# Kernel tuning notes

Hardware: AMD Instinct MI355X
Metric: run time of the kernel (lower is better)

Reference implementation:

```python
import jax, jax.numpy as jnp
import numpy as np

D, H, DK, DF = 512, 8, 64, 2048  # dim, heads, head_dim, forward_dim
EPS = 1e-5


def _layernorm(x, g, b):
    mu = jnp.mean(x, axis=-1, keepdims=True)
    var = jnp.mean(jnp.square(x - mu), axis=-1, keepdims=True)
    return (x - mu) * jax.lax.rsqrt(var + EPS) * g + b


def setup_inputs() -> dict:
    key = jax.random.key(0)
    ks = jax.random.split(key, 16)
    B, S = 2, 2048
    s_in = 1.0 / np.sqrt(D)
    s_ff = 1.0 / np.sqrt(DF)
    s_cat = 1.0 / np.sqrt(H * DK)
    return {
        "x": jax.random.normal(ks[0], (B, S, D), jnp.float32),
        # per-head Q/K/V projections stacked over heads: [H, D, DK]
        "Wq": jax.random.uniform(ks[1], (H, D, DK), jnp.float32, -s_in, s_in),
        "bq": jax.random.uniform(ks[2], (H, DK), jnp.float32, -s_in, s_in),
        "Wk": jax.random.uniform(ks[3], (H, D, DK), jnp.float32, -s_in, s_in),
        "bk": jax.random.uniform(ks[4], (H, DK), jnp.float32, -s_in, s_in),
        "Wv": jax.random.uniform(ks[5], (H, D, DK), jnp.float32, -s_in, s_in),
        "bv": jax.random.uniform(ks[6], (H, DK), jnp.float32, -s_in, s_in),
        "Wo": jax.random.uniform(ks[7], (H * DK, D), jnp.float32, -s_cat, s_cat),
        "bo": jax.random.uniform(ks[8], (D,), jnp.float32, -s_cat, s_cat),
        "ln1_g": jnp.ones((D,), jnp.float32),
        "ln1_b": jnp.zeros((D,), jnp.float32),
        "W1": jax.random.uniform(ks[9], (D, DF), jnp.float32, -s_in, s_in),
        "b1": jax.random.uniform(ks[10], (DF,), jnp.float32, -s_in, s_in),
        "W2": jax.random.uniform(ks[11], (DF, D), jnp.float32, -s_ff, s_ff),
        "b2": jax.random.uniform(ks[12], (D,), jnp.float32, -s_ff, s_ff),
        "ln2_g": jnp.ones((D,), jnp.float32),
        "ln2_b": jnp.zeros((D,), jnp.float32),
    }


def reference(x, Wq, bq, Wk, bk, Wv, bv, Wo, bo, ln1_g, ln1_b, W1, b1, W2, b2, ln2_g, ln2_b):
    # Per-head projections, batched over heads: [B,H,S,DK]
    q = jnp.einsum('bsd,hdk->bhsk', x, Wq) + bq[None, :, None, :]
    k = jnp.einsum('bsd,hdk->bhsk', x, Wk) + bk[None, :, None, :]
    v = jnp.einsum('bsd,hdk->bhsk', x, Wv) + bv[None, :, None, :]
    scale = 1.0 / np.sqrt(DK)
    scores = jnp.einsum('bhsk,bhtk->bhst', q, k) * scale  # [B,H,S,S]
    attn = jax.nn.softmax(scores, axis=-1)
    o = jnp.einsum('bhst,bhtk->bhsk', attn, v)  # [B,H,S,DK]
    # concat heads (head order matches torch cat over ModuleList)
    B, _, S, _ = o.shape
    o = o.transpose(0, 2, 1, 3).reshape(B, S, H * DK)
    attn_out = o @ Wo + bo
    # Residual 1 (dropout = identity in eval): LN(x + sublayer(x))
    h = _layernorm(x + attn_out, ln1_g, ln1_b)
    # FeedForward + Residual 2
    ff = jax.nn.relu(h @ W1 + b1) @ W2 + b2
    return _layernorm(h + ff, ln2_g, ln2_b)
```

## Files before the change

kernel.cpp:

```cpp
#include <hip/hip_runtime.h>


#define Dm   512
#define Hh   8
#define DKk  64
#define DFf  2048
#define Bb   2
#define Ss   2048
#define Nn   4096

typedef __attribute__((ext_vector_type(8))) short short8;
typedef __attribute__((ext_vector_type(4))) float f32x4;
typedef __attribute__((ext_vector_type(4))) short short4v;

__device__ inline float bf2f(short s) {
    unsigned u = ((unsigned)(unsigned short)s) << 16;
    float f; __builtin_memcpy(&f, &u, 4); return f;
}
__device__ inline short f2bf(float f) {
    unsigned u; __builtin_memcpy(&u, &f, 4);
    u = (u + 0x7fff + ((u >> 16) & 1)) >> 16;
    return (short)u;
}
__device__ inline short cvt_elem(const void* p, long i, int f32flag) {
    if (f32flag) return f2bf(((const float*)p)[i]);
    return ((const short*)p)[i];
}
__device__ inline int detect_f32(const void* x) {
    const float* xf = (const float*)x;
    int ok = 0;
#pragma unroll
    for (int i = 0; i < 16; ++i) {
        float a = fabsf(xf[i]);
        ok += (a > 1e-8f && a < 1e4f) ? 1 : 0;
    }
    return ok >= 8;
}
__device__ inline void gload_lds16(const short* g, short* l) {
    __builtin_amdgcn_global_load_lds(
        (const __attribute__((address_space(1))) unsigned int*)g,
        (__attribute__((address_space(3))) unsigned int*)l, 16, 0, 0);
}

__global__ __launch_bounds__(256) void prep_kernel(
    const void* __restrict__ x, short* __restrict__ xb,
    const void* bq, const void* bk, const void* bv, const void* bo,
    const void* b1, const void* b2, const void* g1, const void* be1,
    const void* g2, const void* be2, short* __restrict__ smalls,
    const void* Wq, const void* Wk, const void* Wv,
    const void* Wo, const void* W1, const void* W2,
    short* __restrict__ WqkvT,
    short* __restrict__ WoT, short* __restrict__ W1T, short* __restrict__ W2T)
{
    const int f = detect_f32(x);
    int blk = blockIdx.x;
    if (blk < 512) {
        long base = (long)blk * 4096;
        for (int i = threadIdx.x; i < 4096; i += 256)
            xb[base + i] = cvt_elem(x, base + i, f);
        return;
    }
    if (blk == 512) {
        const void* srcs[10] = {bq, bk, bv, bo, b1, b2, g1, be1, g2, be2};
        const int   sz[10]   = {512, 512, 512, 512, 2048, 512, 512, 512, 512, 512};
        int off = 0;
        for (int j = 0; j < 10; ++j) {
            for (int i = threadIdx.x; i < sz[j]; i += 256)
                smalls[off + i] = cvt_elem(srcs[j], i, f);
            off += sz[j];
        }
        return;
    }
    __shared__ short tile[64][65];
    blk -= 513;
    const void* src; short* dst; long srcoff = 0; long dstoff = 0; int R, C, tr, tc;
    if (blk < 192) {
        int m = blk >> 6; int r = blk & 63; int h = r >> 3; int t = r & 7;
        src = (m == 0) ? Wq : (m == 1) ? Wk : Wv;
        dst = WqkvT + (long)m * 512 * 512;
        srcoff = (long)h * 512 * 64; dstoff = (long)h * 64 * 512;
        R = 512; C = 64; tr = t; tc = 0;
    } else if (blk < 256) {
        int r = blk - 192; src = Wo; dst = WoT; R = 512; C = 512; tr = r >> 3; tc = r & 7;
    } else if (blk < 512) {
        int r = blk - 256; src = W1; dst = W1T; R = 512; C = 2048; tr = r >> 5; tc = r & 31;
    } else {
        int r = blk - 512; src = W2; dst = W2T; R = 2048; C = 512; tr = r >> 3; tc = r & 7;
    }
    int r0 = tr * 64, c0 = tc * 64;
    for (int i = threadIdx.x; i < 4096; i += 256) {
        int rr = i >> 6, cc = i & 63;
        tile[rr][cc] = cvt_elem(src, srcoff + (long)(r0 + rr) * C + c0 + cc, f);
    }
    __syncthreads();
    for (int i = threadIdx.x; i < 4096; i += 256) {
        int cc = i >> 6, rr = i & 63;
        dst[dstoff + (long)(c0 + cc) * R + r0 + rr] = tile[rr][cc];
    }
}

#define MODE_F32       1
#define MODE_RELU_BF16 2
#define MODE_QKV       4

__global__ __launch_bounds__(256) void gemm_kernel(
    const short* __restrict__ A, const short* __restrict__ Bt,
    const short* __restrict__ bias, void* __restrict__ outp,
    void* __restrict__ out2, void* __restrict__ out3,
    int K, int Ncols, int mode, int Ktile)
{
    __shared__ short As[2][128 * 64];
    __shared__ short Bs[2][128 * 64];
    const int t    = threadIdx.x;
    const int lane = t & 63;
    const int wave = t >> 6;
    const int quad = lane >> 4;
    const int l15  = lane & 15;
    const int wm = wave >> 1, wn = wave & 1;
    const int row0 = blockIdx.x * 128;
    const int col0 = blockIdx.y * 128;
    const int kbase = blockIdx.z * Ktile;

    const int ri = lane >> 3;
    const int ct = (lane & 7) ^ ri;

    f32x4 acc[4][4];
#pragma unroll
    for (int i = 0; i < 4; ++i)
#pragma unroll
        for (int j = 0; j < 4; ++j) acc[i][j] = (f32x4){0.f, 0.f, 0.f, 0.f};

    auto stage = [&](int buf, int k0) {
#pragma unroll
        for (int p = 0; p < 4; ++p) {
            int r = wave * 32 + p * 8;
            gload_lds16(A + (long)(row0 + r + ri) * K + kbase + k0 + ct * 8,
                        &As[buf][r * 64 + lane * 8]);
        }
#pragma unroll
        for (int p = 0; p < 4; ++p) {
            int r = wave * 32 + p * 8;
            gload_lds16(Bt + (long)(col0 + r + ri) * K + kbase + k0 + ct * 8,
                        &Bs[buf][r * 64 + lane * 8]);
        }
    };

    stage(0, 0);
    int cur = 0;
    const int niter = Ktile >> 6;
    for (int it = 0; it < niter; ++it) {
        asm volatile("s_waitcnt vmcnt(0)" ::: "memory");
        __syncthreads();
        if (it + 1 < niter) stage(cur ^ 1, (it + 1) * 64);
#pragma unroll
        for (int kk = 0; kk < 2; ++kk) {
            short8 af[4], bfr[4];
#pragma unroll
            for (int mt = 0; mt < 4; ++mt) {
                int rowa = wm * 64 + mt * 16 + l15;
                af[mt] = *(const short8*)&As[cur][rowa * 64
                              + (((kk * 4 + quad) ^ (rowa & 7)) * 8)];
            }
#pragma unroll
            for (int nt = 0; nt < 4; ++nt) {
                int rowb = wn * 64 + nt * 16 + l15;
                bfr[nt] = *(const short8*)&Bs[cur][rowb * 64
                              + (((kk * 4 + quad) ^ (rowb & 7)) * 8)];
            }
#pragma unroll
            for (int mt = 0; mt < 4; ++mt)
#pragma unroll
                for (int nt = 0; nt < 4; ++nt)
                    acc[mt][nt] = __builtin_amdgcn_mfma_f32_16x16x32_bf16(
                        af[mt], bfr[nt], acc[mt][nt], 0, 0, 0);
        }
        cur ^= 1;
    }

    const int wrow0 = row0 + wm * 64;
    const int wcol0 = col0 + wn * 64;
    if (mode == MODE_QKV) {
        int m = wcol0 >> 9;
        if (m < 2) {
            short* out = (short*)(m == 0 ? outp : out2);
#pragma unroll
            for (int nt = 0; nt < 4; ++nt) {
                int col = wcol0 + nt * 16 + l15;
                float bb = bf2f(bias[col]);
                int cl = col & 511;
#pragma unroll
                for (int mt = 0; mt < 4; ++mt)
#pragma unroll
                    for (int r = 0; r < 4; ++r) {
                        int row = wrow0 + mt * 16 + quad * 4 + r;
                        out[(long)row * 512 + cl] = f2bf(acc[mt][nt][r] + bb);
                    }
            }
        } else {
            short* out = (short*)out3;
#pragma unroll
            for (int nt = 0; nt < 4; ++nt) {
                int col = wcol0 + nt * 16 + l15;
                float bb = bf2f(bias[col]);
                int cl = col - 1024;
                int h = cl >> 6, kk = cl & 63;
#pragma unroll
                for (int mt = 0; mt < 4; ++mt)
#pragma unroll
                    for (int r = 0; r < 4; ++r) {
                        int row = wrow0 + mt * 16 + quad * 4 + r;
                        int b = row >> 11, s = row & 2047;
                        out[((long)(b * Hh + h) * DKk + kk) * Ss + s] =
                            f2bf(acc[mt][nt][r] + bb);
                    }
            }
        }
    } else if (mode == MODE_F32) {
        float* out = (float*)outp + (long)blockIdx.z * Nn * Ncols;
        int zb = (blockIdx.z == 0);
#pragma unroll
        for (int nt = 0; nt < 4; ++nt) {
            int col = wcol0 + nt * 16 + l15;
            float bb = zb ? bf2f(bias[col]) : 0.f;
#pragma unroll
            for (int mt = 0; mt < 4; ++mt)
#pragma unroll
                for (int r = 0; r < 4; ++r) {
                    int row = wrow0 + mt * 16 + quad * 4 + r;
                    out[(long)row * Ncols + col] = acc[mt][nt][r] + bb;
                }
        }
    } else {
        short* out = (short*)outp;
#pragma unroll
        for (int nt = 0; nt < 4; ++nt) {
            int col = wcol0 + nt * 16 + l15;
            float bb = bf2f(bias[col]);
#pragma unroll
            for (int mt = 0; mt < 4; ++mt)
#pragma unroll
                for (int r = 0; r < 4; ++r) {
                    int row = wrow0 + mt * 16 + quad * 4 + r;
                    out[(long)row * Ncols + col] = f2bf(fmaxf(acc[mt][nt][r] + bb, 0.f));
                }
        }
    }
}

__global__ __launch_bounds__(256) void attn_kernel(
    const short* __restrict__ Q, const short* __restrict__ Kt,
    const short* __restrict__ Vt, short* __restrict__ po, float* __restrict__ ls)
{
    __shared__ __align__(16) short Ks[2][64 * 64];
    __shared__ __align__(16) short Vs[2][64 * 64];
    __shared__ __align__(16) short pbuf[4][32 * 72];
    const int lane = threadIdx.x & 63;
    const int wave = threadIdx.x >> 6;
    const int quad = lane >> 4;
    const int l15  = lane & 15;
    const int qt = blockIdx.x, bh = blockIdx.y, ks = blockIdx.z;
    const int b = bh >> 3, h = bh & 7;
    const int qrow = b * Ss + qt * 128 + wave * 32;

    short8 aq[2][2];
#pragma unroll
    for (int qh = 0; qh < 2; ++qh)
#pragma unroll
        for (int kk = 0; kk < 2; ++kk)
            aq[qh][kk] = *(const short8*)(Q + (long)(qrow + qh * 16 + l15) * Dm
                                          + h * DKk + kk * 32 + quad * 8);

    f32x4 o[2][4];
    float lsum[2][4];
#pragma unroll
    for (int qh = 0; qh < 2; ++qh) {
#pragma unroll
        for (int nt = 0; nt < 4; ++nt) o[qh][nt] = (f32x4){0.f, 0.f, 0.f, 0.f};
#pragma unroll
        for (int r = 0; r < 4; ++r) lsum[qh][r] = 0.f;
    }

    const short* Kg = Kt + (long)b * Ss * Dm + h * DKk;
    const short* Vg = Vt + (long)bh * DKk * Ss;
    short* pb = pbuf[wave];
    const int t00 = ks * 512;

    const int ri = lane >> 3;
    const int ct = (lane & 7) ^ ri;
    const int ldsrow0 = wave * 16;

    auto stage = [&](int buf, int tkv) {
#pragma unroll
        for (int p = 0; p < 2; ++p) {
            int r = ldsrow0 + p * 8 + ri;
            gload_lds16(Kg + (long)(tkv + r) * Dm + ct * 8,
                        &Ks[buf][(ldsrow0 + p * 8) * 64] + lane * 8);
        }
#pragma unroll
        for (int p = 0; p < 2; ++p) {
            int r = ldsrow0 + p * 8 + ri;
            gload_lds16(Vg + (long)r * Ss + tkv + ct * 8,
                        &Vs[buf][(ldsrow0 + p * 8) * 64] + lane * 8);
        }
    };

    stage(0, t00);
    int cur = 0;
    for (int it = 0; it < 8; ++it) {
        asm volatile("s_waitcnt vmcnt(0)" ::: "memory");
        __syncthreads();
        if (it < 7) stage(cur ^ 1, t00 + (it + 1) * 64);

        f32x4 s[2][4];
#pragma unroll
        for (int j = 0; j < 4; ++j) {
            short8 kf0 = *(const short8*)&Ks[cur][(j * 16 + l15) * 64
                                                  + ((quad) ^ (l15 & 7)) * 8];
            short8 kf1 = *(const short8*)&Ks[cur][(j * 16 + l15) * 64
                                                  + ((4 + quad) ^ (l15 & 7)) * 8];
#pragma unroll
            for (int qh = 0; qh < 2; ++qh) {
                f32x4 sj = (f32x4){0.f, 0.f, 0.f, 0.f};
                sj = __builtin_amdgcn_mfma_f32_16x16x32_bf16(aq[qh][0], kf0, sj, 0, 0, 0);
                sj = __builtin_amdgcn_mfma_f32_16x16x32_bf16(aq[qh][1], kf1, sj, 0, 0, 0);
                s[qh][j] = sj;
            }
        }
#pragma unroll
        for (int qh = 0; qh < 2; ++qh)
#pragma unroll
            for (int j = 0; j < 4; ++j)
#pragma unroll
                for (int r = 0; r < 4; ++r) {
                    float p = __expf(fminf(s[qh][j][r] * 0.125f, 20.f));
                    lsum[qh][r] += p;
                    pb[(qh * 16 + quad * 4 + r) * 72 + j * 16 + l15] = f2bf(p);
                }
        asm volatile("s_waitcnt lgkmcnt(0)" ::: "memory");
#pragma unroll
        for (int c = 0; c < 2; ++c) {
            short8 ap[2];
#pragma unroll
            for (int qh = 0; qh < 2; ++qh)
                ap[qh] = *(const short8*)(pb + (qh * 16 + l15) * 72 + c * 32 + quad * 8);
#pragma unroll
            for (int nt = 0; nt < 4; ++nt) {
                short8 vf = *(const short8*)&Vs[cur][(nt * 16 + l15) * 64
                                                     + ((c * 4 + quad) ^ (l15 & 7)) * 8];
#pragma unroll
                for (int qh = 0; qh < 2; ++qh)
                    o[qh][nt] = __builtin_amdgcn_mfma_f32_16x16x32_bf16(
                        ap[qh], vf, o[qh][nt], 0, 0, 0);
            }
        }
        asm volatile("" ::: "memory");
        cur ^= 1;
    }

#pragma unroll
    for (int qh = 0; qh < 2; ++qh)
#pragma unroll
        for (int r = 0; r < 4; ++r) {
            float v = lsum[qh][r];
            v += __shfl_xor(v, 1);
            v += __shfl_xor(v, 2);
            v += __shfl_xor(v, 4);
            v += __shfl_xor(v, 8);
            lsum[qh][r] = v;
        }
    short* pob = po + ((((long)bh * 16 + qt) * 4 + ks) * 128) * 64;
#pragma unroll
    for (int qh = 0; qh < 2; ++qh)
#pragma unroll
        for (int nt = 0; nt < 4; ++nt)
#pragma unroll
            for (int r = 0; r < 4; ++r)
                pob[(wave * 32 + qh * 16 + quad * 4 + r) * 64 + nt * 16 + l15] =
                    f2bf(o[qh][nt][r]);
    if (l15 == 0) {
        long lbase = (((long)bh * 16 + qt) * 4 + ks) * 128 + wave * 32;
#pragma unroll
        for (int qh = 0; qh < 2; ++qh)
#pragma unroll
            for (int r = 0; r < 4; ++r)
                ls[lbase + qh * 16 + quad * 4 + r] = lsum[qh][r];
    }
}

__global__ __launch_bounds__(256) void combine_kernel(
    const short* __restrict__ po, const float* __restrict__ ls,
    short* __restrict__ O)
{
    const int qt = blockIdx.x, bh = blockIdx.y;
    const int b = bh >> 3, h = bh & 7;
    const long base = ((long)bh * 16 + qt) * 4;
    const int tid = threadIdx.x;
    const int qloc = tid >> 4;
    const int dk0 = (tid & 15) * 4;
#pragma unroll
    for (int q0 = 0; q0 < 8; ++q0) {
        int q = q0 * 16 + qloc;
        f32x4 s = (f32x4){0.f, 0.f, 0.f, 0.f};
        float L = 0.f;
#pragma unroll
        for (int ksp = 0; ksp < 4; ++ksp) {
            short4v pv = *(const short4v*)(po + ((base + ksp) * 128 + q) * 64 + dk0);
#pragma unroll
            for (int i = 0; i < 4; ++i) s[i] += bf2f(pv[i]);
            L += ls[(base + ksp) * 128 + q];
        }
        float inv = 1.f / L;
        short4v ov;
#pragma unroll
        for (int i = 0; i < 4; ++i) ov[i] = f2bf(s[i] * inv);
        *(short4v*)(O + (long)(b * Ss + qt * 128 + q) * Dm + h * DKk + dk0) = ov;
    }
}

__global__ __launch_bounds__(256) void ln_kernel(
    const float* __restrict__ v0, const float* __restrict__ v1,
    const float* __restrict__ v2, const float* __restrict__ v3,
    const short* __restrict__ res,
    const short* __restrict__ g, const short* __restrict__ bt,
    void* __restrict__ out, const void* __restrict__ xdet)
{
    const int row = blockIdx.x, tid = threadIdx.x;
    const long base = (long)row * Dm;
    const long i0 = base + tid, i1 = base + 256 + tid;
    float x0 = v0[i0] + bf2f(res[i0]);
    float x1 = v0[i1] + bf2f(res[i1]);
    if (v1) { x0 += v1[i0]; x1 += v1[i1]; }
    if (v2) { x0 += v2[i0]; x1 += v2[i1]; }
    if (v3) { x0 += v3[i0]; x1 += v3[i1]; }

    __shared__ float red[8];
    const int wv = tid >> 6, ln = tid & 63;
    float s = x0 + x1;
#pragma unroll
    for (int mk = 1; mk < 64; mk <<= 1) s += __shfl_xor(s, mk);
    if (!ln) red[wv] = s;
    __syncthreads();
    float mean = (red[0] + red[1] + red[2] + red[3]) * (1.f / 512.f);
    float d0 = x0 - mean, d1 = x1 - mean;
    float q = d0 * d0 + d1 * d1;
#pragma unroll
    for (int mk = 1; mk < 64; mk <<= 1) q += __shfl_xor(q, mk);
    if (!ln) red[4 + wv] = q;
    __syncthreads();
    float rs = rsqrtf((red[4] + red[5] + red[6] + red[7]) * (1.f / 512.f) + 1e-5f);
    float y0 = d0 * rs * bf2f(g[tid])       + bf2f(bt[tid]);
    float y1 = d1 * rs * bf2f(g[256 + tid]) + bf2f(bt[256 + tid]);
    int f32out = xdet ? detect_f32(xdet) : 0;
    if (f32out) {
        float* o = (float*)out;
        o[i0] = y0; o[i1] = y1;
    } else {
        short* o = (short*)out;
        o[i0] = f2bf(y0); o[i1] = f2bf(y1);
    }
}

extern "C" void kernel_launch(void* const* d_in, const int* in_sizes, int n_in,
                              void* d_out, int out_size, void* d_ws, size_t ws_size,
                              hipStream_t stream)
{
    (void)in_sizes; (void)n_in; (void)out_size; (void)ws_size;
    const void* x   = d_in[0];
    const void* Wq  = d_in[1];  const void* bq  = d_in[2];
    const void* Wk  = d_in[3];  const void* bk  = d_in[4];
    const void* Wv  = d_in[5];  const void* bv  = d_in[6];
    const void* Wo  = d_in[7];  const void* bo  = d_in[8];
    const void* g1  = d_in[9];  const void* be1 = d_in[10];
    const void* W1  = d_in[11]; const void* b1  = d_in[12];
    const void* W2  = d_in[13]; const void* b2  = d_in[14];
    const void* g2  = d_in[15]; const void* be2 = d_in[16];

    char* ws = (char*)d_ws;
    size_t off = 0;
    auto alloc = [&](size_t bytes) -> void* {
        void* p = ws + off; off += (bytes + 255) & ~(size_t)255; return p;
    };
    short* WqkvT = (short*)alloc((size_t)3 * Dm * Dm * 2);
    short* WoT   = (short*)alloc((size_t)Dm * Dm * 2);
    short* W1T   = (short*)alloc((size_t)DFf * Dm * 2);
    short* W2T   = (short*)alloc((size_t)Dm * DFf * 2);
    short* xb    = (short*)alloc((size_t)Nn * Dm * 2);
    short* sm    = (short*)alloc((size_t)6656 * 2);
    char*  regA  = (char*)alloc((size_t)Nn * DFf * 2);
    short* Qb    = (short*)(regA);
    short* Kb    = (short*)(regA + (size_t)Nn * Dm * 2);
    short* Vt    = (short*)(regA + (size_t)Nn * Dm * 4);
    short* Ob    = (short*)(regA + (size_t)Nn * Dm * 6);
    short* u     = (short*)(regA);
    float* wo_p  = (float*)alloc((size_t)2 * Nn * Dm * 4);
    char*  regC  = (char*)alloc((size_t)4 * Nn * Dm * 4);
    short* po    = (short*)regC;
    float* f2p   = (float*)regC;
    float* lsb   = (float*)alloc((size_t)16 * 16 * 4 * 128 * 4);
    short* h_bf  = (short*)alloc((size_t)Nn * Dm * 2);

    prep_kernel<<<1281, 256, 0, stream>>>(x, xb, bq, bk, bv, bo, b1, b2,
                                          g1, be1, g2, be2, sm,
                                          Wq, Wk, Wv, Wo, W1, W2,
                                          WqkvT, WoT, W1T, W2T);
    gemm_kernel<<<dim3(Nn / 128, 1536 / 128, 1), 256, 0, stream>>>(
        xb, WqkvT, sm + 0, Qb, Kb, Vt, Dm, 1536, MODE_QKV, Dm);
    attn_kernel<<<dim3(Ss / 128, Bb * Hh, 4), 256, 0, stream>>>(Qb, Kb, Vt, po, lsb);
    combine_kernel<<<dim3(Ss / 128, Bb * Hh), 256, 0, stream>>>(po, lsb, Ob);
    gemm_kernel<<<dim3(Nn / 128, Dm / 128, 2), 256, 0, stream>>>(
        Ob, WoT, sm + 1536, wo_p, nullptr, nullptr, Dm, Dm, MODE_F32, Dm / 2);
    ln_kernel<<<Nn, 256, 0, stream>>>(wo_p, wo_p + (long)Nn * Dm, nullptr, nullptr,
                                      xb, sm + 4608, sm + 5120, h_bf, nullptr);
    gemm_kernel<<<dim3(Nn / 128, DFf / 128, 1), 256, 0, stream>>>(
        h_bf, W1T, sm + 2048, u, nullptr, nullptr, Dm, DFf, MODE_RELU_BF16, Dm);
    gemm_kernel<<<dim3(Nn / 128, Dm / 128, 4), 256, 0, stream>>>(
        u, W2T, sm + 4096, f2p, nullptr, nullptr, DFf, Dm, MODE_F32, DFf / 4);
    ln_kernel<<<Nn, 256, 0, stream>>>(f2p, f2p + (long)Nn * Dm, f2p + (long)2 * Nn * Dm,
                                      f2p + (long)3 * Nn * Dm,
                                      h_bf, sm + 5632, sm + 6144, d_out, x);
}
```

Measured before the change: 214.6 us.

## Transpose score MFMA, fold Q scale into projection, single-buffer attention LDS

```diff
diff --git a/kernel.cpp b/kernel.cpp
--- a/kernel.cpp
+++ b/kernel.cpp
@@ -12,6 +12,7 @@
 typedef __attribute__((ext_vector_type(8))) short short8;
 typedef __attribute__((ext_vector_type(4))) float f32x4;
 typedef __attribute__((ext_vector_type(4))) short short4v;
+typedef __attribute__((ext_vector_type(2))) int   int2v;
 
 __device__ inline float bf2f(short s) {
     unsigned u = ((unsigned)(unsigned short)s) << 16;
@@ -183,6 +184,7 @@
         int m = wcol0 >> 9;
         if (m < 2) {
             short* out = (short*)(m == 0 ? outp : out2);
+            float sc = (m == 0) ? 0.125f : 1.0f;
 #pragma unroll
             for (int nt = 0; nt < 4; ++nt) {
                 int col = wcol0 + nt * 16 + l15;
@@ -193,7 +195,7 @@
 #pragma unroll
                     for (int r = 0; r < 4; ++r) {
                         int row = wrow0 + mt * 16 + quad * 4 + r;
-                        out[(long)row * 512 + cl] = f2bf(acc[mt][nt][r] + bb);
+                        out[(long)row * 512 + cl] = f2bf((acc[mt][nt][r] + bb) * sc);
                     }
             }
         } else {
@@ -251,8 +253,8 @@
     const short* __restrict__ Q, const short* __restrict__ Kt,
     const short* __restrict__ Vt, short* __restrict__ po, float* __restrict__ ls)
 {
-    __shared__ __align__(16) short Ks[2][64 * 64];
-    __shared__ __align__(16) short Vs[2][64 * 64];
+    __shared__ __align__(16) short Ks[64 * 64];
+    __shared__ __align__(16) short Vs[64 * 64];
     __shared__ __align__(16) short pbuf[4][32 * 72];
     const int lane = threadIdx.x & 63;
     const int wave = threadIdx.x >> 6;
@@ -262,91 +264,83 @@
     const int b = bh >> 3, h = bh & 7;
     const int qrow = b * Ss + qt * 128 + wave * 32;
 
-    short8 aq[2][2];
+    short8 bq[2][2];
 #pragma unroll
     for (int qh = 0; qh < 2; ++qh)
 #pragma unroll
         for (int kk = 0; kk < 2; ++kk)
-            aq[qh][kk] = *(const short8*)(Q + (long)(qrow + qh * 16 + l15) * Dm
+            bq[qh][kk] = *(const short8*)(Q + (long)(qrow + qh * 16 + l15) * Dm
                                           + h * DKk + kk * 32 + quad * 8);
 
     f32x4 o[2][4];
-    float lsum[2][4];
-#pragma unroll
-    for (int qh = 0; qh < 2; ++qh) {
+    float lsum[2] = {0.f, 0.f};
+#pragma unroll
+    for (int qh = 0; qh < 2; ++qh)
 #pragma unroll
         for (int nt = 0; nt < 4; ++nt) o[qh][nt] = (f32x4){0.f, 0.f, 0.f, 0.f};
-#pragma unroll
-        for (int r = 0; r < 4; ++r) lsum[qh][r] = 0.f;
-    }
 
     const short* Kg = Kt + (long)b * Ss * Dm + h * DKk;
     const short* Vg = Vt + (long)bh * DKk * Ss;
-    short* pb = pbuf[wave];
+    short* pbw = pbuf[wave];
     const int t00 = ks * 512;
 
     const int ri = lane >> 3;
     const int ct = (lane & 7) ^ ri;
     const int ldsrow0 = wave * 16;
 
-    auto stage = [&](int buf, int tkv) {
+    for (int it = 0; it < 8; ++it) {
+        const int t0 = t00 + it * 64;
 #pragma unroll
         for (int p = 0; p < 2; ++p) {
             int r = ldsrow0 + p * 8 + ri;
-            gload_lds16(Kg + (long)(tkv + r) * Dm + ct * 8,
-                        &Ks[buf][(ldsrow0 + p * 8) * 64] + lane * 8);
+            gload_lds16(Kg + (long)(t0 + r) * Dm + ct * 8,
+                        &Ks[(ldsrow0 + p * 8) * 64] + lane * 8);
         }
 #pragma unroll
         for (int p = 0; p < 2; ++p) {
             int r = ldsrow0 + p * 8 + ri;
-            gload_lds16(Vg + (long)r * Ss + tkv + ct * 8,
-                        &Vs[buf][(ldsrow0 + p * 8) * 64] + lane * 8);
-        }
-    };
-
-    stage(0, t00);
-    int cur = 0;
-    for (int it = 0; it < 8; ++it) {
+            gload_lds16(Vg + (long)r * Ss + t0 + ct * 8,
+                        &Vs[(ldsrow0 + p * 8) * 64] + lane * 8);
+        }
         asm volatile("s_waitcnt vmcnt(0)" ::: "memory");
         __syncthreads();
-        if (it < 7) stage(cur ^ 1, t00 + (it + 1) * 64);
-
-        f32x4 s[2][4];
+
 #pragma unroll
         for (int j = 0; j < 4; ++j) {
-            short8 kf0 = *(const short8*)&Ks[cur][(j * 16 + l15) * 64
-                                                  + ((quad) ^ (l15 & 7)) * 8];
-            short8 kf1 = *(const short8*)&Ks[cur][(j * 16 + l15) * 64
-                                                  + ((4 + quad) ^ (l15 & 7)) * 8];
+            short8 kf0 = *(const short8*)&Ks[(j * 16 + l15) * 64
+                                             + ((quad ^ (l15 & 7)) * 8)];
+            short8 kf1 = *(const short8*)&Ks[(j * 16 + l15) * 64
+                                             + (((4 + quad) ^ (l15 & 7)) * 8)];
 #pragma unroll
             for (int qh = 0; qh < 2; ++qh) {
                 f32x4 sj = (f32x4){0.f, 0.f, 0.f, 0.f};
-                sj = __builtin_amdgcn_mfma_f32_16x16x32_bf16(aq[qh][0], kf0, sj, 0, 0, 0);
-                sj = __builtin_amdgcn_mfma_f32_16x16x32_bf16(aq[qh][1], kf1, sj, 0, 0, 0);
-                s[qh][j] = sj;
+                sj = __builtin_amdgcn_mfma_f32_16x16x32_bf16(kf0, bq[qh][0], sj, 0, 0, 0);
+                sj = __builtin_amdgcn_mfma_f32_16x16x32_bf16(kf1, bq[qh][1], sj, 0, 0, 0);
+                int2v pk;
+#pragma unroll
+                for (int r2 = 0; r2 < 2; ++r2) {
+                    float pa = __expf(fminf(sj[r2 * 2 + 0], 20.f));
+                    float pc = __expf(fminf(sj[r2 * 2 + 1], 20.f));
+                    lsum[qh] += pa + pc;
+                    unsigned ua, uc;
+                    __builtin_memcpy(&ua, &pa, 4);
+                    __builtin_memcpy(&uc, &pc, 4);
+                    pk[r2] = __builtin_amdgcn_perm(uc, ua, 0x07060302);
+                }
+                *(int2v*)&pbw[(qh * 16 + l15) * 72 + j * 16 + quad * 4] = pk;
             }
         }
-#pragma unroll
-        for (int qh = 0; qh < 2; ++qh)
-#pragma unroll
-            for (int j = 0; j < 4; ++j)
-#pragma unroll
-                for (int r = 0; r < 4; ++r) {
-                    float p = __expf(fminf(s[qh][j][r] * 0.125f, 20.f));
-                    lsum[qh][r] += p;
-                    pb[(qh * 16 + quad * 4 + r) * 72 + j * 16 + l15] = f2bf(p);
-                }
         asm volatile("s_waitcnt lgkmcnt(0)" ::: "memory");
 #pragma unroll
         for (int c = 0; c < 2; ++c) {
             short8 ap[2];
 #pragma unroll
             for (int qh = 0; qh < 2; ++qh)
-                ap[qh] = *(const short8*)(pb + (qh * 16 + l15) * 72 + c * 32 + quad * 8);
+                ap[qh] = *(const short8*)&pbw[(qh * 16 + l15) * 72 + c * 32 + quad * 8];
 #pragma unroll
             for (int nt = 0; nt < 4; ++nt) {
-                short8 vf = *(const short8*)&Vs[cur][(nt * 16 + l15) * 64
-                                                     + ((c * 4 + quad) ^ (l15 & 7)) * 8];
+                short8 vf = *(const short8*)&Vs[(nt * 16 + l15) * 64
+                                                + (((c * 4 + quad) ^ (l15 & 7)) * 8)];
 #pragma unroll
                 for (int qh = 0; qh < 2; ++qh)
                     o[qh][nt] = __builtin_amdgcn_mfma_f32_16x16x32_bf16(
@@ -354,20 +348,16 @@
             }
         }
         asm volatile("" ::: "memory");
-        cur ^= 1;
-    }
-
-#pragma unroll
-    for (int qh = 0; qh < 2; ++qh)
-#pragma unroll
-        for (int r = 0; r < 4; ++r) {
-            float v = lsum[qh][r];
-            v += __shfl_xor(v, 1);
-            v += __shfl_xor(v, 2);
-            v += __shfl_xor(v, 4);
-            v += __shfl_xor(v, 8);
-            lsum[qh][r] = v;
-        }
+        __syncthreads();
+    }
+
+#pragma unroll
+    for (int qh = 0; qh < 2; ++qh) {
+        float v = lsum[qh];
+        v += __shfl_xor(v, 16);
+        v += __shfl_xor(v, 32);
+        lsum[qh] = v;
+    }
     short* pob = po + ((((long)bh * 16 + qt) * 4 + ks) * 128) * 64;
 #pragma unroll
     for (int qh = 0; qh < 2; ++qh)
@@ -377,13 +367,10 @@
             for (int r = 0; r < 4; ++r)
                 pob[(wave * 32 + qh * 16 + quad * 4 + r) * 64 + nt * 16 + l15] =
                     f2bf(o[qh][nt][r]);
-    if (l15 == 0) {
+    if (lane < 16) {
         long lbase = (((long)bh * 16 + qt) * 4 + ks) * 128 + wave * 32;
-#pragma unroll
-        for (int qh = 0; qh < 2; ++qh)
-#pragma unroll
-            for (int r = 0; r < 4; ++r)
-                ls[lbase + qh * 16 + quad * 4 + r] = lsum[qh][r];
+        ls[lbase + l15]      = lsum[0];
+        ls[lbase + 16 + l15] = lsum[1];
     }
 }
 
```

Measured after the change: 209.1 us. 1.03x faster.
